# Kernel optimization log

Measured on AMD Instinct MI355X. Metric: run time of the kernel, lower is better.

Reference implementation:

```python
import jax, jax.numpy as jnp
import numpy as np

B, L, D = 4, 4096, 1024


def hippo_freqs(dim):
    n = np.arange(dim, dtype=np.float32)
    f = np.sqrt(2 * n + 1)
    f = f / f.max()
    return np.exp(-f * np.log(10000)).astype(np.float32)


def setup_inputs() -> dict:
    key = jax.random.key(0)
    ks = jax.random.split(key, 8)
    s = 1.0 / np.sqrt(D)
    return {
        "x": jax.random.normal(ks[0], (B, L, D), dtype=jnp.float32),
        "omega": jnp.asarray(hippo_freqs(D)),
        "log_gamma": jax.random.normal(ks[1], (D,), dtype=jnp.float32) - 3.0,
        "dt": jnp.float32(0.1),
        "W_psi": jax.random.uniform(ks[2], (2 * D, D), jnp.float32, -s, s),
        "b_psi": jax.random.uniform(ks[3], (2 * D,), jnp.float32, -s, s),
        "W_phi": jax.random.uniform(ks[4], (2 * D, D), jnp.float32, -s, s),
        "b_phi": jax.random.uniform(ks[5], (2 * D,), jnp.float32, -s, s),
        "W_gate": jax.random.uniform(ks[6], (D, D), jnp.float32, -s, s),
        "b_gate": jax.random.uniform(ks[7], (D,), jnp.float32, -s, s),
    }


def _proj(z):
    # exact_projection: per-channel-axis standardization over last dim (biased var)
    mean = z.mean(axis=-1, keepdims=True)
    var = ((z - mean) ** 2).mean(axis=-1, keepdims=True)
    return (z - mean) / (jnp.sqrt(var) + 1e-6)


def reference(x, omega, log_gamma, dt, W_psi, b_psi, W_phi, b_phi, W_gate, b_gate):
    Bn, Ln, Dn = x.shape
    psi_raw = jnp.einsum("bld,ed->ble", x, W_psi) + b_psi
    phi_raw = jnp.einsum("bld,ed->ble", x, W_phi) + b_phi
    psi = jax.lax.complex(psi_raw[..., :Dn], psi_raw[..., Dn:])
    phi = jax.lax.complex(phi_raw[..., :Dn], phi_raw[..., Dn:])
    gate = jax.nn.sigmoid(jnp.einsum("bld,ed->ble", x, W_gate) + b_gate)
    U = gate.astype(psi.dtype) * psi  # [B,L,D] complex

    dt_abs = jnp.abs(dt)
    lam = jax.lax.complex(-jnp.exp(log_gamma), omega)  # [D]
    t_axis = jnp.arange(Ln, dtype=jnp.float32)
    kernel = jnp.exp(lam[None, :] * t_axis[:, None].astype(lam.dtype) * dt_abs)  # [L,D]

    n_fft = 2 * Ln
    Kf = jnp.fft.fft(kernel, n=n_fft, axis=0)          # [2L,D]
    Uf = jnp.fft.fft(U, n=n_fft, axis=1)               # [B,2L,D]
    H = jnp.fft.ifft(Uf * Kf[None], axis=1)[:, :Ln]    # causal conv, [B,L,D]

    H_proj = jax.lax.complex(_proj(H.real), _proj(H.imag))
    return (H_proj * jnp.conj(phi)).real
```

## Files before the change

### kernel.cpp

```cpp
#include <hip/hip_runtime.h>
#include <hip/hip_bf16.h>
#include <math.h>

#define B_ 4
#define L_ 4096
#define D_ 1024
#define M_ (B_*L_)
#define N_ 5120
#define K_ 1024
#define CHUNKS 128
#define LC 32
#define PL ((long)M_ * D_)

#define WS_NEEDED 211812352ull

typedef __attribute__((ext_vector_type(8))) short bf16x8;
typedef __attribute__((ext_vector_type(4))) float f32x4;

__device__ inline float b2f(short s) {
    unsigned u = ((unsigned)(unsigned short)s) << 16;
    float f; __builtin_memcpy(&f, &u, 4); return f;
}

__device__ inline void cvt4(const float4* __restrict__ src, ushort* __restrict__ dst, long j) {
    float4 v = src[j];
    __hip_bfloat16 a = __float2bfloat16(v.x), b = __float2bfloat16(v.y),
                   c = __float2bfloat16(v.z), d = __float2bfloat16(v.w);
    ushort4 o = { *(ushort*)&a, *(ushort*)&b, *(ushort*)&c, *(ushort*)&d };
    *(ushort4*)(dst + j * 4) = o;
}

__global__ void convert_kernel(const float* __restrict__ x,
                               const float* __restrict__ Wpsi,
                               const float* __restrict__ Wphi,
                               const float* __restrict__ Wgate,
                               ushort* __restrict__ xb,
                               ushort* __restrict__ wb) {
    long i0 = (long)blockIdx.x * blockDim.x + threadIdx.x;
    long stride = (long)gridDim.x * blockDim.x;
    const long nx4 = ((long)M_ * K_) >> 2;
    for (long j = i0; j < nx4; j += stride) cvt4((const float4*)x, xb, j);
    const long nW14 = (2048L * 1024) >> 2, nW34 = (1024L * 1024) >> 2;
    for (long j = i0; j < nW14; j += stride) cvt4((const float4*)Wpsi, wb, j);
    for (long j = i0; j < nW14; j += stride) cvt4((const float4*)Wphi, wb + 2048L * 1024, j);
    for (long j = i0; j < nW34; j += stride) cvt4((const float4*)Wgate, wb + 4096L * 1024, j);
}

#define BM2 256
#define BN2 256
#define BK2 64
#define NT  (K_ / BK2)
#define DBUF_BYTES 65536

#define STAGE(gptr, brow, kt, slotoff)                                                       \
  do {                                                                                       \
    const __hip_bfloat16* g0_ = (gptr) + (long)((brow) + srow0) * K_ + (kt) * 64 + sgc0 * 8; \
    const __hip_bfloat16* g1_ = (gptr) + (long)((brow) + srow1) * K_ + (kt) * 64 + sgc1 * 8; \
    __builtin_amdgcn_global_load_lds((const __attribute__((address_space(1))) void*)g0_,     \
        (__attribute__((address_space(3))) void*)(smem + (slotoff) + ldst0), 16, 0, 0);      \
    __builtin_amdgcn_global_load_lds((const __attribute__((address_space(1))) void*)g1_,     \
        (__attribute__((address_space(3))) void*)(smem + (slotoff) + ldst1), 16, 0, 0);      \
  } while (0)

#define RDA1(db, qm, i_)                                                            \
  do {                                                                              \
    aA[i_][0] = *(const bf16x8*)((db) + aoff + (qm) * 8192 + (i_) * 2048 + ct0);    \
    aA[i_][1] = *(const bf16x8*)((db) + aoff + (qm) * 8192 + (i_) * 2048 + ct1);    \
  } while (0)
#define RDB1(db, qn, s, j_)                                                         \
  do {                                                                              \
    bB[s][j_][0] = *(const bf16x8*)((db) + boff + (qn) * 4096 + (j_) * 2048 + ct0); \
    bB[s][j_][1] = *(const bf16x8*)((db) + boff + (qn) * 4096 + (j_) * 2048 + ct1); \
  } while (0)

#define MFMA16(qm, qn, s)                                                                         \
  _Pragma("unroll") for (int i_ = 0; i_ < 4; ++i_)                                                \
    _Pragma("unroll") for (int j_ = 0; j_ < 2; ++j_) {                                            \
      acc[(qm)*4+i_][(qn)*2+j_] = __builtin_amdgcn_mfma_f32_16x16x32_bf16(                        \
          aA[i_][0], bB[s][j_][0], acc[(qm)*4+i_][(qn)*2+j_], 0, 0, 0);                           \
      acc[(qm)*4+i_][(qn)*2+j_] = __builtin_amdgcn_mfma_f32_16x16x32_bf16(                        \
          aA[i_][1], bB[s][j_][1], acc[(qm)*4+i_][(qn)*2+j_], 0, 0, 0);                           \
    }
#define BARRIER __builtin_amdgcn_s_barrier()

__global__ __launch_bounds__(512, 2)
void gemm_kernel(const __hip_bfloat16* __restrict__ xb,
                 const __hip_bfloat16* __restrict__ wb,
                 const float* __restrict__ b_psi,
                 const float* __restrict__ b_phi,
                 const float* __restrict__ b_gate,
                 __hip_bfloat16* __restrict__ raw5) {
    __shared__ __attribute__((aligned(16))) char smem[2 * DBUF_BYTES];

    const int tid   = threadIdx.x;
    const int wid   = tid >> 6;
    const int lane  = tid & 63;
    const int row16 = lane & 15;
    const int quad  = lane >> 4;
    const int wm    = wid >> 2;
    const int wn    = wid & 3;

    const int bid = blockIdx.y * 64 + blockIdx.x;
    const int swz = (bid & 7) * (1280 / 8) + (bid >> 3);
    const int m_blk = (swz & 63) * BM2;
    const int n_blk = (swz >> 6) * BN2;

    const int srow0 = tid >> 3;
    const int srow1 = (512 + tid) >> 3;
    const int sch   = tid & 7;
    const int sgc0  = sch ^ (srow0 & 7);
    const int sgc1  = sch ^ (srow1 & 7);
    const int ldst0 = (wid * 64) * 16;
    const int ldst1 = (512 + wid * 64) * 16;

    const int sw   = row16 & 7;
    const int aoff = wm * 16384 + row16 * 128;
    const int boff = 32768 + (wn >> 1) * 16384 + ((wn & 1) * 64 + row16) * 128;
    const int ct0  = ((0 * 4 + quad) ^ sw) * 16;
    const int ct1  = ((1 * 4 + quad) ^ sw) * 16;

    bf16x8 aA[4][2];
    bf16x8 bB[2][2][2];
    f32x4  acc[8][4] = {};

    STAGE(xb, m_blk,       0, 0);
    STAGE(xb, m_blk + 128, 0, 16384);
    STAGE(wb, n_blk,       0, 32768);
    STAGE(wb, n_blk + 128, 0, 32768 + 16384);
    STAGE(wb, n_blk,       1, DBUF_BYTES + 32768);
    STAGE(wb, n_blk + 128, 1, DBUF_BYTES + 32768 + 16384);
    asm volatile("s_waitcnt vmcnt(4)" ::: "memory");
    BARRIER;

    for (int t = 0; t < NT; ++t) {
        char* db = smem + (t & 1) * DBUF_BYTES;
        const int nb = ((t + 1) & 1) * DBUF_BYTES;
        const int cb = (t & 1) * DBUF_BYTES;
        RDA1(db, 0, 0); RDB1(db, 0, 0, 0); RDB1(db, 0, 0, 1);
        RDA1(db, 0, 1); RDA1(db, 0, 2); RDA1(db, 0, 3);
        if (t + 1 < NT) STAGE(xb, m_blk, t + 1, nb);
        BARRIER;
        __builtin_amdgcn_s_setprio(1); MFMA16(0, 0, 0); __builtin_amdgcn_s_setprio(0);
        BARRIER;
        RDB1(db, 1, 1, 0); RDB1(db, 1, 1, 1);
        if (t + 1 < NT) STAGE(xb, m_blk + 128, t + 1, nb + 16384);
        BARRIER;
        __builtin_amdgcn_s_setprio(1); MFMA16(0, 1, 1); __builtin_amdgcn_s_setprio(0);
        BARRIER;
        RDA1(db, 1, 0); RDA1(db, 1, 1); RDA1(db, 1, 2); RDA1(db, 1, 3);
        if (t + 2 < NT) STAGE(wb, n_blk, t + 2, cb + 32768);
        BARRIER;
        __builtin_amdgcn_s_setprio(1); MFMA16(1, 1, 1); __builtin_amdgcn_s_setprio(0);
        BARRIER;
        if (t + 2 < NT) STAGE(wb, n_blk + 128, t + 2, cb + 32768 + 16384);
        BARRIER;
        __builtin_amdgcn_s_setprio(1); MFMA16(1, 0, 0); __builtin_amdgcn_s_setprio(0);
        if (t < NT - 2) { asm volatile("s_waitcnt vmcnt(4)" ::: "memory"); }
        else            { asm volatile("s_waitcnt vmcnt(0)" ::: "memory"); }
        BARRIER;
    }

#pragma unroll
    for (int mi = 0; mi < 8; ++mi) {
        const int mbase = m_blk + wm * 128 + (mi >> 2) * 64 + (mi & 3) * 16 + quad * 4;
#pragma unroll
        for (int nj = 0; nj < 4; ++nj) {
            int n = n_blk + wn * 64 + (nj >> 1) * 32 + (nj & 1) * 16 + row16;
            float bias = (n < 2048) ? b_psi[n] : (n < 4096) ? b_phi[n - 2048] : b_gate[n - 4096];
            int g = n >> 10, d = n & 1023;
            __hip_bfloat16* pl = raw5 + (long)g * PL;
#pragma unroll
            for (int r = 0; r < 4; ++r)
                pl[(long)(mbase + r) * D_ + d] = __float2bfloat16(acc[mi][nj][r] + bias);
        }
    }
}

__global__ __launch_bounds__(1024) void scan1_kernel(__hip_bfloat16* raw5,
                                                     const float* __restrict__ omega,
                                                     const float* __restrict__ log_gamma,
                                                     const float* __restrict__ dtp,
                                                     float2* __restrict__ E) {
    const int d = threadIdx.x;
    const int c = blockIdx.x;
    const int b = blockIdx.y;
    const float dt = fabsf(dtp[0]);
    const float decay = expf(-expf(log_gamma[d]) * dt);
    const float ang = omega[d] * dt;
    const float ar = decay * cosf(ang), ai = decay * sinf(ang);

    __hip_bfloat16* Pre = raw5;
    __hip_bfloat16* Pim = raw5 + PL;
    const __hip_bfloat16* Gt = raw5 + 4 * PL;
    long base = (long)(b * L_ + c * LC) * D_ + d;

    float hr = 0.f, hi = 0.f;
    for (int i = 0; i < LC; i++) {
        long idx = base + (long)i * D_;
        float sg = 1.f / (1.f + expf(-__bfloat162float(Gt[idx])));
        float ur = sg * __bfloat162float(Pre[idx]);
        float ui = sg * __bfloat162float(Pim[idx]);
        float nhr = ar * hr - ai * hi + ur;
        float nhi = ar * hi + ai * hr + ui;
        hr = nhr; hi = nhi;
        Pre[idx] = __float2bfloat16(hr);
        Pim[idx] = __float2bfloat16(hi);
    }
    E[((long)c * B_ + b) * D_ + d] = make_float2(hr, hi);
}

__global__ void apow_kernel(const float* __restrict__ omega,
                            const float* __restrict__ log_gamma,
                            const float* __restrict__ dtp,
                            float2* __restrict__ apow) {
    int t = blockIdx.x * blockDim.x + threadIdx.x;
    int i = t >> 10, d = t & 1023;
    float dt = fabsf(dtp[0]);
    float e = expf(-expf(log_gamma[d]) * dt * (float)(i + 1));
    float ang = omega[d] * dt * (float)(i + 1);
    apow[t] = make_float2(e * cosf(ang), e * sinf(ang));
}

__global__ __launch_bounds__(128) void carry_kernel(const float2* __restrict__ E,
                                                    const float* __restrict__ omega,
                                                    const float* __restrict__ log_gamma,
                                                    const float* __restrict__ dtp,
                                                    float2* __restrict__ carry) {
    __shared__ float2 sh[CHUNKS];
    const int c = threadIdx.x;
    const int bd = blockIdx.x;
    const int b = bd >> 10, d = bd & 1023;
    const float dt = fabsf(dtp[0]);
    const float gd = expf(log_gamma[d]);
    const float wd = omega[d];

    float2 v = E[((long)c * B_ + b) * D_ + d];
    sh[c] = v;
    __syncthreads();
#pragma unroll
    for (int s = 1; s < CHUNKS; s <<= 1) {
        float2 prev;
        bool has = (c >= s);
        if (has) prev = sh[c - s];
        __syncthreads();
        if (has) {
            float t = dt * (float)LC * (float)s;
            float dec = expf(-gd * t);
            float ang = wd * t;
            float Ar = dec * cosf(ang), Ai = dec * sinf(ang);
            v.x += Ar * prev.x - Ai * prev.y;
            v.y += Ar * prev.y + Ai * prev.x;
            sh[c] = v;
        }
        __syncthreads();
    }
    float2 outv = (c == 0) ? make_float2(0.f, 0.f) : sh[c - 1];
    carry[((long)c * B_ + b) * D_ + d] = outv;
}

__global__ __launch_bounds__(256) void finish_kernel(const __hip_bfloat16* __restrict__ raw5,
                                                     const float2* __restrict__ carry,
                                                     const float2* __restrict__ apow,
                                                     float* __restrict__ out) {
    const int wv = threadIdx.x >> 6, lane = threadIdx.x & 63;
    const int r = blockIdx.x * 4 + wv;
    const int l = r & (L_ - 1);
    const int b = r >> 12;
    const int c = l >> 5, i = l & 31;
    const int d0 = lane * 16;
    const long base = (long)r * D_ + d0;

    const __hip_bfloat16* Hre = raw5;
    const __hip_bfloat16* Him = raw5 + PL;
    const __hip_bfloat16* Pre = raw5 + 2 * PL;
    const __hip_bfloat16* Pim = raw5 + 3 * PL;
    const float2* cr = carry + ((long)c * B_ + b) * D_ + d0;
    const float2* ap = apow + (long)i * D_ + d0;

    bf16x8 hre[2], him[2];
    hre[0] = *(const bf16x8*)(Hre + base);     hre[1] = *(const bf16x8*)(Hre + base + 8);
    him[0] = *(const bf16x8*)(Him + base);     him[1] = *(const bf16x8*)(Him + base + 8);

    float hr[16], hi[16];
    float s0 = 0.f, s1 = 0.f, s2 = 0.f, s3 = 0.f;
#pragma unroll
    for (int j = 0; j < 16; j++) {
        float2 cv = cr[j];
        float2 av = ap[j];
        float fr = av.x * cv.x - av.y * cv.y;
        float fi = av.x * cv.y + av.y * cv.x;
        float xr = b2f(hre[j >> 3][j & 7]) + fr;
        float xi = b2f(him[j >> 3][j & 7]) + fi;
        hr[j] = xr; hi[j] = xi;
        s0 += xr; s1 += xr * xr; s2 += xi; s3 += xi * xi;
    }
#pragma unroll
    for (int m = 1; m < 64; m <<= 1) {
        s0 += __shfl_xor(s0, m);
        s1 += __shfl_xor(s1, m);
        s2 += __shfl_xor(s2, m);
        s3 += __shfl_xor(s3, m);
    }
    float mean_r = s0 * (1.f / D_);
    float var_r  = s1 * (1.f / D_) - mean_r * mean_r;
    float mean_i = s2 * (1.f / D_);
    float var_i  = s3 * (1.f / D_) - mean_i * mean_i;
    float inv_r = 1.f / (sqrtf(fmaxf(var_r, 0.f)) + 1e-6f);
    float inv_i = 1.f / (sqrtf(fmaxf(var_i, 0.f)) + 1e-6f);

    bf16x8 pre[2], pim[2];
    pre[0] = *(const bf16x8*)(Pre + base);     pre[1] = *(const bf16x8*)(Pre + base + 8);
    pim[0] = *(const bf16x8*)(Pim + base);     pim[1] = *(const bf16x8*)(Pim + base + 8);

    float o[16];
#pragma unroll
    for (int j = 0; j < 16; j++)
        o[j] = (hr[j] - mean_r) * inv_r * b2f(pre[j >> 3][j & 7])
             + (hi[j] - mean_i) * inv_i * b2f(pim[j >> 3][j & 7]);
#pragma unroll
    for (int q = 0; q < 4; q++)
        *(float4*)(out + base + q * 4) = make_float4(o[q*4], o[q*4+1], o[q*4+2], o[q*4+3]);
}

extern "C" void kernel_launch(void* const* d_in, const int* in_sizes, int n_in,
                              void* d_out, int out_size, void* d_ws, size_t ws_size,
                              hipStream_t stream) {
    (void)in_sizes; (void)n_in; (void)out_size;
    if (ws_size < WS_NEEDED) return;

    const float* x         = (const float*)d_in[0];
    const float* omega     = (const float*)d_in[1];
    const float* log_gamma = (const float*)d_in[2];
    const float* dt        = (const float*)d_in[3];
    const float* W_psi     = (const float*)d_in[4];
    const float* b_psi     = (const float*)d_in[5];
    const float* W_phi     = (const float*)d_in[6];
    const float* b_phi     = (const float*)d_in[7];
    const float* W_gate    = (const float*)d_in[8];
    const float* b_gate    = (const float*)d_in[9];

    char* ws = (char*)d_ws;
    __hip_bfloat16* xb   = (__hip_bfloat16*)(ws);
    __hip_bfloat16* wb   = (__hip_bfloat16*)(ws + 33554432);
    __hip_bfloat16* raw5 = (__hip_bfloat16*)(ws + 44040192);
    float2* E     = (float2*)(ws);
    float2* carry = (float2*)(ws + 4194304);
    float2* apow  = (float2*)(ws + 8388608);
    float* out = (float*)d_out;

    convert_kernel<<<2048, 256, 0, stream>>>(x, W_psi, W_phi, W_gate, (ushort*)xb, (ushort*)wb);
    gemm_kernel<<<dim3(M_ / BM2, N_ / BN2), 512, 0, stream>>>(xb, wb, b_psi, b_phi, b_gate, raw5);
    apow_kernel<<<128, 256, 0, stream>>>(omega, log_gamma, dt, apow);
    scan1_kernel<<<dim3(CHUNKS, B_), 1024, 0, stream>>>(raw5, omega, log_gamma, dt, E);
    carry_kernel<<<B_ * D_, 128, 0, stream>>>(E, omega, log_gamma, dt, carry);
    finish_kernel<<<M_ / 4, 256, 0, stream>>>(raw5, carry, apow, out);
}
```

Before: 445.8 us.

## Simplify GEMM main loop to plain double-buffered prefetch with one barrier

Replaces the interleaved multi-barrier schedule, which staged A one tile ahead and B two tiles ahead, with a plain double buffer. All four tiles for step t+1 are issued at the top of the iteration, the whole tile is computed, then the loop waits on vmcnt(0) and one barrier. The aim is to remove the per-iteration barriers and priority toggles. In exchange, loads are less finely interleaved with MFMA work and the B prefetch distance drops to one tile, so memory latency may be exposed more.

```diff
diff --git a/kernel.cpp b/kernel.cpp
--- a/kernel.cpp
+++ b/kernel.cpp
@@ -83,6 +83,18 @@
     }
 #define BARRIER __builtin_amdgcn_s_barrier()
 
+#define COMPUTE_TILE(db)                                                                          \
+  do {                                                                                            \
+    RDA1(db, 0, 0); RDB1(db, 0, 0, 0); RDB1(db, 0, 0, 1);                                         \
+    RDA1(db, 0, 1); RDA1(db, 0, 2); RDA1(db, 0, 3);                                               \
+    __builtin_amdgcn_s_setprio(1); MFMA16(0, 0, 0); __builtin_amdgcn_s_setprio(0);                \
+    RDB1(db, 1, 1, 0); RDB1(db, 1, 1, 1);                                                         \
+    __builtin_amdgcn_s_setprio(1); MFMA16(0, 1, 1); __builtin_amdgcn_s_setprio(0);                \
+    RDA1(db, 1, 0); RDA1(db, 1, 1); RDA1(db, 1, 2); RDA1(db, 1, 3);                               \
+    __builtin_amdgcn_s_setprio(1); MFMA16(1, 1, 1); MFMA16(1, 0, 0);                              \
+    __builtin_amdgcn_s_setprio(0);                                                                \
+  } while (0)
+
 __global__ __launch_bounds__(512, 2)
 void gemm_kernel(const __hip_bfloat16* __restrict__ xb,
                  const __hip_bfloat16* __restrict__ wb,
@@ -127,37 +139,23 @@
     STAGE(xb, m_blk + 128, 0, 16384);
     STAGE(wb, n_blk,       0, 32768);
     STAGE(wb, n_blk + 128, 0, 32768 + 16384);
-    STAGE(wb, n_blk,       1, DBUF_BYTES + 32768);
-    STAGE(wb, n_blk + 128, 1, DBUF_BYTES + 32768 + 16384);
-    asm volatile("s_waitcnt vmcnt(4)" ::: "memory");
+    asm volatile("s_waitcnt vmcnt(0)" ::: "memory");
     BARRIER;
 
-    for (int t = 0; t < NT; ++t) {
+    for (int t = 0; t < NT - 1; ++t) {
         char* db = smem + (t & 1) * DBUF_BYTES;
         const int nb = ((t + 1) & 1) * DBUF_BYTES;
-        const int cb = (t & 1) * DBUF_BYTES;
-        RDA1(db, 0, 0); RDB1(db, 0, 0, 0); RDB1(db, 0, 0, 1);
-        RDA1(db, 0, 1); RDA1(db, 0, 2); RDA1(db, 0, 3);
-        if (t + 1 < NT) STAGE(xb, m_blk, t + 1, nb);
+        STAGE(xb, m_blk,       t + 1, nb);
+        STAGE(xb, m_blk + 128, t + 1, nb + 16384);
+        STAGE(wb, n_blk,       t + 1, nb + 32768);
+        STAGE(wb, n_blk + 128, t + 1, nb + 32768 + 16384);
+        COMPUTE_TILE(db);
+        asm volatile("s_waitcnt vmcnt(0)" ::: "memory");
         BARRIER;
-        __builtin_amdgcn_s_setprio(1); MFMA16(0, 0, 0); __builtin_amdgcn_s_setprio(0);
-        BARRIER;
-        RDB1(db, 1, 1, 0); RDB1(db, 1, 1, 1);
-        if (t + 1 < NT) STAGE(xb, m_blk + 128, t + 1, nb + 16384);
-        BARRIER;
-        __builtin_amdgcn_s_setprio(1); MFMA16(0, 1, 1); __builtin_amdgcn_s_setprio(0);
-        BARRIER;
-        RDA1(db, 1, 0); RDA1(db, 1, 1); RDA1(db, 1, 2); RDA1(db, 1, 3);
-        if (t + 2 < NT) STAGE(wb, n_blk, t + 2, cb + 32768);
-        BARRIER;
-        __builtin_amdgcn_s_setprio(1); MFMA16(1, 1, 1); __builtin_amdgcn_s_setprio(0);
-        BARRIER;
-        if (t + 2 < NT) STAGE(wb, n_blk + 128, t + 2, cb + 32768 + 16384);
-        BARRIER;
-        __builtin_amdgcn_s_setprio(1); MFMA16(1, 0, 0); __builtin_amdgcn_s_setprio(0);
-        if (t < NT - 2) { asm volatile("s_waitcnt vmcnt(4)" ::: "memory"); }
-        else            { asm volatile("s_waitcnt vmcnt(0)" ::: "memory"); }
-        BARRIER;
+    }
+    {
+        char* db = smem + ((NT - 1) & 1) * DBUF_BYTES;
+        COMPUTE_TILE(db);
     }
 
 #pragma unroll
```

Measured after the change: 441.3 us. No clear change (-1.0%).
